# Optimization experiments

Measured on AMD Instinct MI355X. Metric: run time of the kernel, lower is better.

## Reference

```python
import jax, jax.numpy as jnp
import numpy as np

IN_CH = 256
NUM_CLASSES = 1
CONF_THR = 0.3
NMS_IOU = 0.2
ANCHOR_SIZES = (32.0, 64.0, 128.0)
ASPECTS = (0.5, 1.0, 2.0)
NUM_ANCHORS = len(ANCHOR_SIZES) * len(ASPECTS)  # 9
K_CAND = 1024   # top-score candidates fed to NMS per image
MAX_DET = 100   # max_output_size in source
BN_EPS = 1e-5


def _anchors():
    a = [[s * r / 224.0, s / r / 224.0] for s in ANCHOR_SIZES for r in ASPECTS]
    return jnp.asarray(a, jnp.float32)  # [A, 2] (w, h)


def _conv(x, w, b, pad):
    y = jax.lax.conv_general_dilated(x, w, (1, 1), [(pad, pad), (pad, pad)],
                                     dimension_numbers=('NCHW', 'OIHW', 'NCHW'))
    return y + b[None, :, None, None]


def _bn(x, g, b, m, v):
    inv = jax.lax.rsqrt(v + BN_EPS)
    return (x - m[None, :, None, None]) * (g * inv)[None, :, None, None] + b[None, :, None, None]


def _corners(b):
    return (b[..., 0] - b[..., 2] / 2, b[..., 1] - b[..., 3] / 2,
            b[..., 0] + b[..., 2] / 2, b[..., 1] + b[..., 3] / 2)


def _iou_one(box, boxes):
    # box: [4] cxcywh, boxes: [K,4] -> iou [K]
    ax1, ay1, ax2, ay2 = _corners(box)
    bx1, by1, bx2, by2 = _corners(boxes)
    iw = jnp.maximum(jnp.minimum(ax2, bx2) - jnp.maximum(ax1, bx1), 0.0)
    ih = jnp.maximum(jnp.minimum(ay2, by2) - jnp.maximum(ay1, by1), 0.0)
    inter = iw * ih
    union = (ax2 - ax1) * (ay2 - ay1) + (bx2 - bx1) * (by2 - by1) - inter
    return inter / (union + 1e-16)


def _nms(boxes, scores):
    # boxes [K,4], scores [K] -> kept boxes padded to [MAX_DET,4]
    s0 = jnp.where(scores > CONF_THR, scores, -1.0)

    def body(i, carry):
        s, out = carry
        j = jnp.argmax(s)
        ok = s[j] > 0.0
        box = boxes[j]
        iou = _iou_one(box, boxes)
        s_new = jnp.where(iou > NMS_IOU, -1.0, s).at[j].set(-1.0)
        s = jnp.where(ok, s_new, s)
        out = out.at[i].set(jnp.where(ok, box, jnp.zeros_like(box)))
        return s, out

    _, out = jax.lax.fori_loop(0, MAX_DET, body,
                               (s0, jnp.zeros((MAX_DET, 4), boxes.dtype)))
    return out


def _forward(features, w1, b1, g1, be1, m1, v1, w2, b2, g2, be2, m2, v2, wo, bo):
    x = jax.nn.relu(_bn(_conv(features, w1, b1, 1), g1, be1, m1, v1))
    x = jax.nn.relu(_bn(_conv(x, w2, b2, 1), g2, be2, m2, v2))
    p = _conv(x, wo, bo, 0)                      # [B, A*(5+C), H, W]
    B, _, H, W = p.shape
    p = p.reshape(B, NUM_ANCHORS, 5 + NUM_CLASSES, H, W).transpose(0, 3, 4, 1, 2)  # [B,H,W,A,5+C]
    obj = jax.nn.sigmoid(p[..., 4])
    anch = _anchors()
    gx = jnp.arange(W, dtype=p.dtype)[None, :, None]
    gy = jnp.arange(H, dtype=p.dtype)[:, None, None]
    px = (jax.nn.sigmoid(p[..., 0]) + gx) / W
    py = (jax.nn.sigmoid(p[..., 1]) + gy) / H
    pw = jnp.exp(p[..., 2]) * anch[:, 0]
    ph = jnp.exp(p[..., 3]) * anch[:, 1]
    boxes = jnp.stack([px, py, pw, ph], -1).reshape(B, -1, 4)
    if NUM_CLASSES > 1:
        scores = obj * jax.nn.sigmoid(p[..., 5:]).max(-1)
    else:
        scores = obj
    scores = scores.reshape(B, -1)

    def per_image(bx, sc):
        top_s, idx = jax.lax.top_k(sc, K_CAND)
        return _nms(bx[idx], top_s)

    return jax.vmap(per_image)(boxes, scores)    # [B, MAX_DET, 4]


def setup_inputs() -> dict:
    key = jax.random.key(0)
    ks = jax.random.split(key, 16)
    B = 32
    c1, c2 = IN_CH // 2, IN_CH // 4
    oc = NUM_ANCHORS * (5 + NUM_CLASSES)
    return {
        'features': jax.random.normal(ks[0], (B, IN_CH, 56, 56), jnp.float32),
        'w1': jax.random.normal(ks[1], (c1, IN_CH, 3, 3), jnp.float32) * 0.02,
        'b1': jax.random.normal(ks[2], (c1,), jnp.float32) * 0.02,
        'g1': 1.0 + 0.1 * jax.random.normal(ks[3], (c1,), jnp.float32),
        'be1': 0.1 * jax.random.normal(ks[4], (c1,), jnp.float32),
        'm1': 0.1 * jax.random.normal(ks[5], (c1,), jnp.float32),
        'v1': jax.random.uniform(ks[6], (c1,), jnp.float32, 0.5, 1.5),
        'w2': jax.random.normal(ks[7], (c2, c1, 3, 3), jnp.float32) * 0.03,
        'b2': jax.random.normal(ks[8], (c2,), jnp.float32) * 0.02,
        'g2': 1.0 + 0.1 * jax.random.normal(ks[9], (c2,), jnp.float32),
        'be2': 0.1 * jax.random.normal(ks[10], (c2,), jnp.float32),
        'm2': 0.1 * jax.random.normal(ks[11], (c2,), jnp.float32),
        'v2': jax.random.uniform(ks[12], (c2,), jnp.float32, 0.5, 1.5),
        'wo': jax.random.normal(ks[13], (oc, c2, 1, 1), jnp.float32) * 0.1,
        'bo': jax.random.normal(ks[14], (oc,), jnp.float32) * 0.05,
    }


def reference(features, w1, b1, g1, be1, m1, v1, w2, b2, g2, be2, m2, v2, wo, bo):
    return _forward(features, w1, b1, g1, be1, m1, v1, w2, b2, g2, be2, m2, v2, wo, bo)
```

## Files before the change

kernel.cpp:

```cpp
#include <hip/hip_runtime.h>
#include <math.h>
#include <stdint.h>

constexpr int BB   = 32;
constexpr int HW   = 3136;
constexpr int C0   = 256, C1 = 128, C2 = 64;
constexpr int NA   = 9;
constexpr int NCAND = HW * NA;
constexpr int KSEL  = 1024;
constexpr int MAXDET = 100;

typedef _Float16 half8 __attribute__((ext_vector_type(8)));
typedef _Float16 half4v __attribute__((ext_vector_type(4)));
typedef float    f32x4  __attribute__((ext_vector_type(4)));
typedef float    f32x16 __attribute__((ext_vector_type(16)));

__device__ __forceinline__ void g2l16(const void* g, void* l) {
    auto gp = reinterpret_cast<const __attribute__((address_space(1))) char*>(
        reinterpret_cast<uintptr_t>(g));
    auto lp = reinterpret_cast<__attribute__((address_space(3))) char*>(
        reinterpret_cast<uintptr_t>(l));
    __builtin_amdgcn_global_load_lds(gp, lp, 16, 0, 0);
}

__global__ void bn_prep(const float* __restrict__ g, const float* __restrict__ be,
                        const float* __restrict__ m, const float* __restrict__ v,
                        const float* __restrict__ cb,
                        float* __restrict__ scl, float* __restrict__ tb, int n) {
    int i = threadIdx.x;
    if (i < n) {
        float inv = 1.f / sqrtf(v[i] + 1e-5f);
        float s = g[i] * inv;
        scl[i] = s;
        tb[i] = be[i] + (cb[i] - m[i]) * s;
    }
}

__global__ void reorder_w6(const float* __restrict__ w, _Float16* __restrict__ wc,
                           int CIN, int COUT) {
    int i = blockIdx.x * 256 + threadIdx.x;
    int K = CIN * 9;
    if (i >= 2 * COUT * K) return;
    int ci  = i & 31;
    int row = (i >> 5) % (2 * COUT);
    int ch  = (i >> 5) / (2 * COUT);
    int pl  = row / COUT;
    int oc  = row - pl * COUT;
    int cg = ch / 9, r = ch - cg * 9;
    int cin = cg * 32 + ci;
    float v = w[oc * K + cin * 9 + r];
    _Float16 h = (_Float16)v;
    wc[i] = pl ? (_Float16)(v - (float)h) : h;
}

__global__ __launch_bounds__(256) void nchw_to_nhwc_split(
    const float* __restrict__ in, _Float16* __restrict__ hi, _Float16* __restrict__ lo)
{
    __shared__ float tile[64 * 68];
    const int pt = blockIdx.x * 64, ct = blockIdx.y * 64, b = blockIdx.z;
    const int t = threadIdx.x;
    const int r0 = t >> 4, cidx = (t & 15) * 4;
#pragma unroll
    for (int rr = 0; rr < 64; rr += 16) {
        int r = rr + r0;
        const float* src = in + ((size_t)(b * 256 + ct + r)) * HW + pt + cidx;
        float4 v = *(const float4*)src;
        float* d = &tile[r * 68 + cidx];
        d[0] = v.x; d[1] = v.y; d[2] = v.z; d[3] = v.w;
    }
    __syncthreads();
    const int p = t >> 2, c0 = (t & 3) * 16;
    size_t obase = ((size_t)(b * HW + pt + p)) * 256 + ct + c0;
    half8 h0, h1, l0, l1;
#pragma unroll
    for (int j = 0; j < 16; ++j) {
        float v = tile[(c0 + j) * 68 + p];
        _Float16 hh = (_Float16)v;
        _Float16 ll = (_Float16)(v - (float)hh);
        if (j < 8) { h0[j] = hh; l0[j] = ll; }
        else       { h1[j - 8] = hh; l1[j - 8] = ll; }
    }
    *(half8*)(hi + obase)     = h0;
    *(half8*)(hi + obase + 8) = h1;
    *(half8*)(lo + obase)     = l0;
    *(half8*)(lo + obase + 8) = l1;
}

template <int CIN, int COUT, int MINW, bool NHWC_OUT>
__global__ __launch_bounds__(256, MINW) void conv3x3_v10(
    const _Float16* __restrict__ xhi,
    const _Float16* __restrict__ xlo,
    const _Float16* __restrict__ wc,
    const _Float16* __restrict__ zbuf,
    const float* __restrict__ scl, const float* __restrict__ tb,
    _Float16* __restrict__ ohi,
    _Float16* __restrict__ olo,
    float* __restrict__ onchw)
{
    constexpr int K       = CIN * 9;
    constexpr int NCH     = K / 32;
    constexpr int WROWS   = 2 * COUT;
    constexpr int CHALVES = WROWS * 32;
    constexpr int WI      = WROWS / 64;
    constexpr int PI      = 2;
    constexpr int WOC     = COUT / 64;

    __shared__ __align__(16) _Float16 SP[128 * 64];
    __shared__ __align__(16) _Float16 SW[WROWS * 32];

    const int bid = blockIdx.x;
    const int swz = (bid & 7) * (gridDim.x >> 3) + (bid >> 3);
    const int b = swz / 25;
    const int pixBase = (swz - b * 25) * 128;
    const int bHW = b * HW;

    const int t = threadIdx.x, l = t & 63, w = t >> 6;

    const int cpix = (l & 7) ^ ((l >> 3) & 7);
    const int ppl = cpix >> 2, pq = cpix & 3;
    const _Float16* xsp = ppl ? xlo : xhi;
    int py[4], px[4];
    const _Float16* pbase[4];
#pragma unroll
    for (int i = 0; i < 4; ++i) {
        int p = w * 32 + i * 8 + (l >> 3);
        int pix = pixBase + p;
        py[i] = pix / 56; px[i] = pix - py[i] * 56;
        pbase[i] = xsp + (size_t)(bHW + pix) * CIN + pq * 8;
    }
    const int cw = (l & 3) ^ ((l >> 3) & 3);
    const _Float16* wbase = wc + ((size_t)(w * (WI * 16) + (l >> 2))) * 32 + cw * 8;

    const int wid = t >> 6;
    const int wp = wid & 1, wo = wid >> 1;
    const int lc = l & 31, lk = l >> 5;

    f32x16 acc[PI][WOC];
#pragma unroll
    for (int pi = 0; pi < PI; ++pi)
#pragma unroll
        for (int oi = 0; oi < WOC; ++oi) acc[pi][oi] = (f32x16)0.f;

    auto stage = [&](int ch) {
        int cg = ch / 9, r = ch - cg * 9;
        int ky = r / 3;
        int dy = ky - 1, dx = (r - ky * 3) - 1;
        int off = (dy * 56 + dx) * CIN + cg * 32;
#pragma unroll
        for (int i = 0; i < 4; ++i) {
            bool v = ((unsigned)(py[i] + dy) < 56u) && ((unsigned)(px[i] + dx) < 56u);
            const void* src = v ? (const void*)(pbase[i] + off) : (const void*)zbuf;
            g2l16(src, (void*)&SP[w * 2048 + i * 512]);
        }
        const _Float16* wsrc = wbase + (size_t)ch * CHALVES;
#pragma unroll
        for (int j = 0; j < WI; ++j)
            g2l16((const void*)(wsrc + j * 512), (void*)&SW[(w * WI + j) * 512]);
    };

    auto compute = [&]() {
#pragma unroll
        for (int ks = 0; ks < 2; ++ks) {
            half8 pb[PI][2];
#pragma unroll
            for (int pi = 0; pi < PI; ++pi) {
                int prw = wp * (PI * 32) + pi * 32 + lc;
                int key = prw & 7;
#pragma unroll
                for (int pl2 = 0; pl2 < 2; ++pl2) {
                    int c = pl2 * 4 + ks * 2 + lk;
                    pb[pi][pl2] = *(const half8*)&SP[prw * 64 + ((c ^ key) << 3)];
                }
            }
            half8 wa[WOC][2];
#pragma unroll
            for (int oi = 0; oi < WOC; ++oi)
#pragma unroll
                for (int pl2 = 0; pl2 < 2; ++pl2) {
                    int row = pl2 * COUT + wo * (WOC * 32) + oi * 32 + lc;
                    int c = ks * 2 + lk;
                    wa[oi][pl2] = *(const half8*)&SW[row * 32 + ((c ^ ((row >> 1) & 3)) << 3)];
                }
#pragma unroll
            for (int pi = 0; pi < PI; ++pi)
#pragma unroll
                for (int oi = 0; oi < WOC; ++oi) {
                    acc[pi][oi] = __builtin_amdgcn_mfma_f32_32x32x16_f16(wa[oi][0], pb[pi][0], acc[pi][oi], 0, 0, 0);
                    acc[pi][oi] = __builtin_amdgcn_mfma_f32_32x32x16_f16(wa[oi][0], pb[pi][1], acc[pi][oi], 0, 0, 0);
                    acc[pi][oi] = __builtin_amdgcn_mfma_f32_32x32x16_f16(wa[oi][1], pb[pi][0], acc[pi][oi], 0, 0, 0);
                }
        }
    };

    for (int ch = 0; ch < NCH; ++ch) {
        stage(ch);
        __syncthreads();
        compute();
        __syncthreads();
    }

#pragma unroll
    for (int pi = 0; pi < PI; ++pi) {
        const int pix = pixBase + wp * (PI * 32) + pi * 32 + lc;
        if (pix < HW) {
#pragma unroll
            for (int oi = 0; oi < WOC; ++oi) {
#pragma unroll
                for (int g = 0; g < 4; ++g) {
                    const int oc0 = wo * (WOC * 32) + oi * 32 + 8 * g + 4 * lk;
                    f32x4 s4 = *(const f32x4*)(scl + oc0);
                    f32x4 t4 = *(const f32x4*)(tb + oc0);
                    if constexpr (NHWC_OUT) {
                        half4v hh, ll;
#pragma unroll
                        for (int m2 = 0; m2 < 4; ++m2) {
                            float val = fmaxf(acc[pi][oi][g * 4 + m2] * s4[m2] + t4[m2], 0.f);
                            _Float16 h = (_Float16)val;
                            hh[m2] = h;
                            ll[m2] = (_Float16)(val - (float)h);
                        }
                        size_t o = ((size_t)(bHW + pix)) * COUT + oc0;
                        *(half4v*)(ohi + o) = hh;
                        *(half4v*)(olo + o) = ll;
                    } else {
#pragma unroll
                        for (int m2 = 0; m2 < 4; ++m2) {
                            float val = fmaxf(acc[pi][oi][g * 4 + m2] * s4[m2] + t4[m2], 0.f);
                            onchw[((size_t)(b * COUT + oc0 + m2)) * HW + pix] = val;
                        }
                    }
                }
            }
        }
    }
}

__global__ __launch_bounds__(256) void conv1x1_decode(
    const float* __restrict__ x2, const float* __restrict__ wo,
    const float* __restrict__ bo,
    float* __restrict__ boxes, float* __restrict__ scores)
{
    __shared__ float ws[64 * 56];
    for (int i = threadIdx.x; i < 54 * 64; i += 256) {
        int oc = i % 54, c = i / 54;
        ws[c * 56 + oc] = wo[oc * 64 + c];
    }
    __syncthreads();

    int u = blockIdx.x * 256 + threadIdx.x;
    int a = u % 9;
    int rest = u / 9;
    int quad = rest % 784;
    int b = rest / 784;
    int pix0 = quad * 4;
    int y = pix0 / 56;
    int x0 = pix0 - y * 56;

    const float* xb = x2 + (size_t)b * 64 * HW + pix0;
    float acc[5][4];
#pragma unroll
    for (int j = 0; j < 5; ++j)
#pragma unroll
        for (int p = 0; p < 4; ++p) acc[j][p] = 0.f;

#pragma unroll 8
    for (int c = 0; c < 64; ++c) {
        float4 xv = *(const float4*)(xb + c * HW);
#pragma unroll
        for (int j = 0; j < 5; ++j) {
            float w = ws[c * 56 + a * 6 + j];
            acc[j][0] += w * xv.x;
            acc[j][1] += w * xv.y;
            acc[j][2] += w * xv.z;
            acc[j][3] += w * xv.w;
        }
    }

    int si = a / 3, ri = a - si * 3;
    float sv = (float)(32 << si);
    float rv = 0.5f * (float)(1 << ri);
    float aw = (sv * rv) / 224.f;
    float ah = (sv / rv) / 224.f;
    float bo0 = bo[a * 6 + 0], bo1 = bo[a * 6 + 1], bo2 = bo[a * 6 + 2];
    float bo3 = bo[a * 6 + 3], bo4 = bo[a * 6 + 4];

#pragma unroll
    for (int p = 0; p < 4; ++p) {
        float p0 = acc[0][p] + bo0;
        float p1 = acc[1][p] + bo1;
        float p2 = acc[2][p] + bo2;
        float p3 = acc[3][p] + bo3;
        float p4 = acc[4][p] + bo4;
        float sx = 1.f / (1.f + expf(-p0));
        float sy = 1.f / (1.f + expf(-p1));
        float pxc = (sx + (float)(x0 + p)) / 56.f;
        float pyc = (sy + (float)y) / 56.f;
        float pw = expf(p2) * aw;
        float ph = expf(p3) * ah;
        float sc = 1.f / (1.f + expf(-p4));
        int n = (y * 56 + x0 + p) * 9 + a;
        float4 bx; bx.x = pxc; bx.y = pyc; bx.z = pw; bx.w = ph;
        *(float4*)&boxes[((size_t)b * NCAND + n) * 4] = bx;
        scores[(size_t)b * NCAND + n] = sc;
    }
}

__device__ __forceinline__ unsigned fkey(float f) {
    unsigned u = __float_as_uint(f);
    return (u & 0x80000000u) ? ~u : (u | 0x80000000u);
}

__global__ __launch_bounds__(1024) void topk_select(
    const float* __restrict__ scores, const float* __restrict__ boxes,
    float* __restrict__ cbox, float* __restrict__ csc, int* __restrict__ cidx)
{
    const int b = blockIdx.x, t = threadIdx.x;
    const float* sp = scores + (size_t)b * NCAND;
    const int lane = t & 63, w = t >> 6;

    __shared__ unsigned hist[256];
    __shared__ unsigned wsum[16];
    __shared__ unsigned s_sel, s_need, s_tot0, s_tot1;

    unsigned prefix = 0, maskSo = 0;
    int need = KSEL;

    for (int round = 0; round < 4; ++round) {
        int shift = 24 - round * 8;
        if (t < 256) hist[t] = 0;
        __syncthreads();
        for (int i = t; i < NCAND; i += 1024) {
            unsigned u = fkey(sp[i]);
            if ((u & maskSo) == prefix) atomicAdd(&hist[(u >> shift) & 255], 1u);
        }
        __syncthreads();
        if (t == 0) {
            int rem = need;
            unsigned sel = 0;
            for (int v = 255; v >= 0; --v) {
                int c = (int)hist[v];
                if (c >= rem) { sel = (unsigned)v; break; }
                rem -= c;
            }
            s_sel = sel; s_need = (unsigned)rem;
        }
        __syncthreads();
        prefix |= (s_sel << shift);
        maskSo |= (0xFFu << shift);
        need = (int)s_need;
        __syncthreads();
    }

    const unsigned cutoff = prefix;
    const unsigned needT = (unsigned)need;
    unsigned outBase = 0, tieBase = 0;
    const unsigned long long mlt = (1ull << lane) - 1ull;

    for (int c0 = 0; c0 < NCAND; c0 += 1024) {
        int i = c0 + t;
        bool valid = i < NCAND;
        float sc = valid ? sp[i] : 0.f;
        unsigned u = valid ? fkey(sc) : 0u;
        bool gt = valid && (u > cutoff);
        bool eq = valid && (u == cutoff);

        unsigned long long balE = __ballot(eq);
        unsigned lpE = (unsigned)__popcll(balE & mlt);
        if (lane == 0) wsum[w] = (unsigned)__popcll(balE);
        __syncthreads();
        if (t == 0) {
            unsigned run = 0;
            for (int k = 0; k < 16; ++k) { unsigned x = wsum[k]; wsum[k] = run; run += x; }
            s_tot1 = run;
        }
        __syncthreads();
        unsigned tieRank = tieBase + wsum[w] + lpE;
        bool take = gt || (eq && tieRank < needT);
        __syncthreads();

        unsigned long long balT = __ballot(take);
        unsigned lpT = (unsigned)__popcll(balT & mlt);
        if (lane == 0) wsum[w] = (unsigned)__popcll(balT);
        __syncthreads();
        if (t == 0) {
            unsigned run = 0;
            for (int k = 0; k < 16; ++k) { unsigned x = wsum[k]; wsum[k] = run; run += x; }
            s_tot0 = run;
        }
        __syncthreads();
        unsigned pos = outBase + wsum[w] + lpT;
        if (take) {
            float4 bx = *(const float4*)&boxes[((size_t)b * NCAND + i) * 4];
            *(float4*)&cbox[((size_t)b * KSEL + pos) * 4] = bx;
            csc[(size_t)b * KSEL + pos] = sc;
            cidx[(size_t)b * KSEL + pos] = i;
        }
        tieBase += s_tot1;
        outBase += s_tot0;
        __syncthreads();
    }
}

__global__ __launch_bounds__(64) void nms_wave(
    const float* __restrict__ cbox, const float* __restrict__ csc,
    const int* __restrict__ cidx, float* __restrict__ out)
{
    const int b = blockIdx.x, l = threadIdx.x;
    float cx[16], cy[16], w_[16], h_[16], s[16];
    int id[16];
#pragma unroll
    for (int j = 0; j < 16; ++j) {
        int ci = (b << 10) + (j << 6) + l;
        float4 bb = *(const float4*)&cbox[(size_t)ci * 4];
        float sc = csc[ci];
        cx[j] = bb.x; cy[j] = bb.y; w_[j] = bb.z; h_[j] = bb.w;
        s[j] = sc > 0.3f ? sc : -1.f;
        id[j] = cidx[ci];
    }
    float* ob = out + (size_t)b * MAXDET * 4;

    for (int it = 0; it < MAXDET; ++it) {
        float bs = s[0]; int bi = id[0];
        float bcx = cx[0], bcy = cy[0], bw = w_[0], bh = h_[0];
#pragma unroll
        for (int j = 1; j < 16; ++j) {
            bool tk = (s[j] > bs) || (s[j] == bs && id[j] < bi);
            if (tk) { bs = s[j]; bi = id[j]; bcx = cx[j]; bcy = cy[j]; bw = w_[j]; bh = h_[j]; }
        }
#pragma unroll
        for (int m2 = 1; m2 < 64; m2 <<= 1) {
            float os = __shfl_xor(bs, m2); int oi = __shfl_xor(bi, m2);
            float ox = __shfl_xor(bcx, m2), oy = __shfl_xor(bcy, m2);
            float ow = __shfl_xor(bw, m2), oh2 = __shfl_xor(bh, m2);
            bool tk = (os > bs) || (os == bs && oi < bi);
            if (tk) { bs = os; bi = oi; bcx = ox; bcy = oy; bw = ow; bh = oh2; }
        }
        if (bs <= 0.f) {
            for (int q = it * 4 + l; q < MAXDET * 4; q += 64) ob[q] = 0.f;
            break;
        }
        if (l == 0) {
            float4 o; o.x = bcx; o.y = bcy; o.z = bw; o.w = bh;
            *(float4*)&ob[it * 4] = o;
        }
        float wx1 = bcx - bw / 2.f, wy1 = bcy - bh / 2.f;
        float wx2 = bcx + bw / 2.f, wy2 = bcy + bh / 2.f;
        float war = (wx2 - wx1) * (wy2 - wy1);
#pragma unroll
        for (int j = 0; j < 16; ++j) {
            float jx1 = cx[j] - w_[j] / 2.f, jy1 = cy[j] - h_[j] / 2.f;
            float jx2 = cx[j] + w_[j] / 2.f, jy2 = cy[j] + h_[j] / 2.f;
            float iw = fminf(wx2, jx2) - fmaxf(wx1, jx1); iw = fmaxf(iw, 0.f);
            float ih = fminf(wy2, jy2) - fmaxf(wy1, jy1); ih = fmaxf(ih, 0.f);
            float inter = iw * ih;
            float jar = (jx2 - jx1) * (jy2 - jy1);
            float uni = war + jar - inter;
            if (inter / (uni + 1e-16f) > 0.2f) s[j] = -1.f;
        }
    }
}

extern "C" void kernel_launch(void* const* d_in, const int* in_sizes, int n_in,
                              void* d_out, int out_size, void* d_ws, size_t ws_size,
                              hipStream_t stream)
{
    const float* features = (const float*)d_in[0];
    const float* w1 = (const float*)d_in[1];
    const float* b1 = (const float*)d_in[2];
    const float* g1 = (const float*)d_in[3];
    const float* be1 = (const float*)d_in[4];
    const float* m1 = (const float*)d_in[5];
    const float* v1 = (const float*)d_in[6];
    const float* w2 = (const float*)d_in[7];
    const float* b2 = (const float*)d_in[8];
    const float* g2 = (const float*)d_in[9];
    const float* be2 = (const float*)d_in[10];
    const float* m2 = (const float*)d_in[11];
    const float* v2 = (const float*)d_in[12];
    const float* wo = (const float*)d_in[13];
    const float* bo = (const float*)d_in[14];

    char* ws = (char*)d_ws;
    size_t off = 0;
    auto alloc = [&](size_t bytes) {
        char* p = ws + off;
        off += (bytes + 255) / 256 * 256;
        return p;
    };

    _Float16* zbuf = (_Float16*)alloc(256);
    _Float16* w1c = (_Float16*)alloc((size_t)2 * C1 * 2304 * 2);
    _Float16* w2c = (_Float16*)alloc((size_t)2 * C2 * 1152 * 2);
    float* scl1 = (float*)alloc(C1 * 4);
    float* tb1  = (float*)alloc(C1 * 4);
    float* scl2 = (float*)alloc(C2 * 4);
    float* tb2  = (float*)alloc(C2 * 4);

    const size_t planeF = (size_t)BB * HW * C0 * 2;
    char* regB = alloc(2 * planeF);
    _Float16* fhi = (_Float16*)regB;
    _Float16* flo = (_Float16*)(regB + planeF);

    const size_t planeX1 = (size_t)BB * HW * C1 * 2;
    char* regC = alloc(2 * planeX1);
    _Float16* x1hi = (_Float16*)regC;
    _Float16* x1lo = (_Float16*)(regC + planeX1);

    float* x2     = (float*)regB;
    float* boxes  = (float*)(regB + 25690112);
    float* scores = (float*)(regB + 25690112 + 14450688);
    float* cbox = (float*)regC;
    float* csc  = (float*)(regC + 524288);
    int*   cidx = (int*)(regC + 524288 + 131072);

    hipMemsetAsync(zbuf, 0, 256, stream);
    bn_prep<<<1, 256, 0, stream>>>(g1, be1, m1, v1, b1, scl1, tb1, C1);
    bn_prep<<<1, 256, 0, stream>>>(g2, be2, m2, v2, b2, scl2, tb2, C2);
    reorder_w6<<<(2 * C1 * 2304 + 255) / 256, 256, 0, stream>>>(w1, w1c, C0, C1);
    reorder_w6<<<(2 * C2 * 1152 + 255) / 256, 256, 0, stream>>>(w2, w2c, C1, C2);

    nchw_to_nhwc_split<<<dim3(49, 4, BB), 256, 0, stream>>>(features, fhi, flo);

    conv3x3_v10<C0, C1, 4, true><<<800, 256, 0, stream>>>(
        fhi, flo, w1c, zbuf, scl1, tb1, x1hi, x1lo, nullptr);
    conv3x3_v10<C1, C2, 4, false><<<800, 256, 0, stream>>>(
        x1hi, x1lo, w2c, zbuf, scl2, tb2, nullptr, nullptr, x2);

    conv1x1_decode<<<(BB * 784 * NA) / 256, 256, 0, stream>>>(x2, wo, bo, boxes, scores);

    topk_select<<<BB, 1024, 0, stream>>>(scores, boxes, cbox, csc, cidx);
    nms_wave<<<BB, 64, 0, stream>>>(cbox, csc, cidx, (float*)d_out);
}
```

Before: 650.1 us.

## Use atomic compaction and warp-aggregated histograms in top-k select, merge prep kernels

```diff
diff --git a/kernel.cpp b/kernel.cpp
--- a/kernel.cpp
+++ b/kernel.cpp
@@ -23,24 +23,29 @@
     __builtin_amdgcn_global_load_lds(gp, lp, 16, 0, 0);
 }
 
-__global__ void bn_prep(const float* __restrict__ g, const float* __restrict__ be,
-                        const float* __restrict__ m, const float* __restrict__ v,
-                        const float* __restrict__ cb,
-                        float* __restrict__ scl, float* __restrict__ tb, int n) {
+__global__ void bn_prep2(const float* g1, const float* be1, const float* m1,
+                         const float* v1, const float* cb1,
+                         const float* g2, const float* be2, const float* m2,
+                         const float* v2, const float* cb2,
+                         float* scl1, float* tb1, float* scl2, float* tb2) {
     int i = threadIdx.x;
-    if (i < n) {
-        float inv = 1.f / sqrtf(v[i] + 1e-5f);
-        float s = g[i] * inv;
-        scl[i] = s;
-        tb[i] = be[i] + (cb[i] - m[i]) * s;
-    }
-}
-
-__global__ void reorder_w6(const float* __restrict__ w, _Float16* __restrict__ wc,
-                           int CIN, int COUT) {
-    int i = blockIdx.x * 256 + threadIdx.x;
+    if (i < C1) {
+        float inv = 1.f / sqrtf(v1[i] + 1e-5f);
+        float s = g1[i] * inv;
+        scl1[i] = s;
+        tb1[i] = be1[i] + (cb1[i] - m1[i]) * s;
+    }
+    if (i < C2) {
+        float inv = 1.f / sqrtf(v2[i] + 1e-5f);
+        float s = g2[i] * inv;
+        scl2[i] = s;
+        tb2[i] = be2[i] + (cb2[i] - m2[i]) * s;
+    }
+}
+
+__device__ __forceinline__ void reorder_one(const float* w, _Float16* wc,
+                                            int i, int CIN, int COUT) {
     int K = CIN * 9;
-    if (i >= 2 * COUT * K) return;
     int ci  = i & 31;
     int row = (i >> 5) % (2 * COUT);
     int ch  = (i >> 5) / (2 * COUT);
@@ -51,6 +56,15 @@
     float v = w[oc * K + cin * 9 + r];
     _Float16 h = (_Float16)v;
     wc[i] = pl ? (_Float16)(v - (float)h) : h;
+}
+
+__global__ void reorder_w_both(const float* __restrict__ w1, _Float16* __restrict__ w1c,
+                               const float* __restrict__ w2, _Float16* __restrict__ w2c) {
+    constexpr int N1 = 2 * C1 * C0 * 9;
+    constexpr int N2 = 2 * C2 * C1 * 9;
+    int i = blockIdx.x * 256 + threadIdx.x;
+    if (i < N1) reorder_one(w1, w1c, i, C0, C1);
+    else if (i < N1 + N2) reorder_one(w2, w2c, i - N1, C1, C2);
 }
 
 __global__ __launch_bounds__(256) void nchw_to_nhwc_split(
@@ -312,7 +326,8 @@
 
 __global__ __launch_bounds__(1024) void topk_select(
     const float* __restrict__ scores, const float* __restrict__ boxes,
-    float* __restrict__ cbox, float* __restrict__ csc, int* __restrict__ cidx)
+    float* __restrict__ cbox, float* __restrict__ csc, int* __restrict__ cidx,
+    int* __restrict__ ctrs)
 {
     const int b = blockIdx.x, t = threadIdx.x;
     const float* sp = scores + (size_t)b * NCAND;
@@ -320,7 +335,7 @@
 
     __shared__ unsigned hist[256];
     __shared__ unsigned wsum[16];
-    __shared__ unsigned s_sel, s_need, s_tot0, s_tot1;
+    __shared__ unsigned s_sel, s_need, s_tot1;
 
     unsigned prefix = 0, maskSo = 0;
     int need = KSEL;
@@ -329,9 +344,19 @@
         int shift = 24 - round * 8;
         if (t < 256) hist[t] = 0;
         __syncthreads();
-        for (int i = t; i < NCAND; i += 1024) {
-            unsigned u = fkey(sp[i]);
-            if ((u & maskSo) == prefix) atomicAdd(&hist[(u >> shift) & 255], 1u);
+        for (int i = t; i < NCAND + (1024 - NCAND % 1024); i += 1024) {
+            bool pred = i < NCAND;
+            unsigned u = pred ? fkey(sp[i]) : 0u;
+            pred = pred && ((u & maskSo) == prefix);
+            unsigned bin = (u >> shift) & 255;
+            unsigned long long active = __ballot(pred);
+            while (active) {
+                int leader = __ffsll((unsigned long long)active) - 1;
+                unsigned bl = __shfl(bin, leader);
+                unsigned long long match = __ballot(pred && bin == bl);
+                if (lane == leader) atomicAdd(&hist[bl], (unsigned)__popcll(match));
+                active &= ~match;
+            }
         }
         __syncthreads();
         if (t == 0) {
@@ -353,19 +378,26 @@
 
     const unsigned cutoff = prefix;
     const unsigned needT = (unsigned)need;
-    unsigned outBase = 0, tieBase = 0;
     const unsigned long long mlt = (1ull << lane) - 1ull;
 
+    for (int i = t; i < NCAND; i += 1024) {
+        unsigned u = fkey(sp[i]);
+        if (u > cutoff) {
+            int pos = atomicAdd(&ctrs[b], 1);
+            float4 bx = *(const float4*)&boxes[((size_t)b * NCAND + i) * 4];
+            *(float4*)&cbox[((size_t)b * KSEL + pos) * 4] = bx;
+            csc[(size_t)b * KSEL + pos] = sp[i];
+            cidx[(size_t)b * KSEL + pos] = i;
+        }
+    }
+
+    unsigned tieBase = 0;
     for (int c0 = 0; c0 < NCAND; c0 += 1024) {
         int i = c0 + t;
         bool valid = i < NCAND;
         float sc = valid ? sp[i] : 0.f;
-        unsigned u = valid ? fkey(sc) : 0u;
-        bool gt = valid && (u > cutoff);
-        bool eq = valid && (u == cutoff);
-
+        bool eq = valid && (fkey(sc) == cutoff);
         unsigned long long balE = __ballot(eq);
-        unsigned lpE = (unsigned)__popcll(balE & mlt);
         if (lane == 0) wsum[w] = (unsigned)__popcll(balE);
         __syncthreads();
         if (t == 0) {
@@ -374,30 +406,17 @@
             s_tot1 = run;
         }
         __syncthreads();
-        unsigned tieRank = tieBase + wsum[w] + lpE;
-        bool take = gt || (eq && tieRank < needT);
-        __syncthreads();
-
-        unsigned long long balT = __ballot(take);
-        unsigned lpT = (unsigned)__popcll(balT & mlt);
-        if (lane == 0) wsum[w] = (unsigned)__popcll(balT);
-        __syncthreads();
-        if (t == 0) {
-            unsigned run = 0;
-            for (int k = 0; k < 16; ++k) { unsigned x = wsum[k]; wsum[k] = run; run += x; }
-            s_tot0 = run;
-        }
-        __syncthreads();
-        unsigned pos = outBase + wsum[w] + lpT;
-        if (take) {
+        unsigned rank = tieBase + wsum[w] + (unsigned)__popcll(balE & mlt);
+        if (eq && rank < needT) {
+            int pos = atomicAdd(&ctrs[b], 1);
             float4 bx = *(const float4*)&boxes[((size_t)b * NCAND + i) * 4];
             *(float4*)&cbox[((size_t)b * KSEL + pos) * 4] = bx;
             csc[(size_t)b * KSEL + pos] = sc;
             cidx[(size_t)b * KSEL + pos] = i;
         }
         tieBase += s_tot1;
-        outBase += s_tot0;
-        __syncthreads();
+        __syncthreads();
+        if (tieBase >= needT) break;
     }
 }
 
@@ -489,6 +508,7 @@
     };
 
     _Float16* zbuf = (_Float16*)alloc(256);
+    int* ctrs = (int*)alloc(BB * 4);
     _Float16* w1c = (_Float16*)alloc((size_t)2 * C1 * 2304 * 2);
     _Float16* w2c = (_Float16*)alloc((size_t)2 * C2 * 1152 * 2);
     float* scl1 = (float*)alloc(C1 * 4);
@@ -514,10 +534,13 @@
     int*   cidx = (int*)(regC + 524288 + 131072);
 
     hipMemsetAsync(zbuf, 0, 256, stream);
-    bn_prep<<<1, 256, 0, stream>>>(g1, be1, m1, v1, b1, scl1, tb1, C1);
-    bn_prep<<<1, 256, 0, stream>>>(g2, be2, m2, v2, b2, scl2, tb2, C2);
-    reorder_w6<<<(2 * C1 * 2304 + 255) / 256, 256, 0, stream>>>(w1, w1c, C0, C1);
-    reorder_w6<<<(2 * C2 * 1152 + 255) / 256, 256, 0, stream>>>(w2, w2c, C1, C2);
+    hipMemsetAsync(ctrs, 0, BB * 4, stream);
+    bn_prep2<<<1, 256, 0, stream>>>(g1, be1, m1, v1, b1, g2, be2, m2, v2, b2,
+                                    scl1, tb1, scl2, tb2);
+    {
+        int total = 2 * C1 * 2304 + 2 * C2 * 1152;
+        reorder_w_both<<<(total + 255) / 256, 256, 0, stream>>>(w1, w1c, w2, w2c);
+    }
 
     nchw_to_nhwc_split<<<dim3(49, 4, BB), 256, 0, stream>>>(features, fhi, flo);
 
@@ -528,6 +551,6 @@
 
     conv1x1_decode<<<(BB * 784 * NA) / 256, 256, 0, stream>>>(x2, wo, bo, boxes, scores);
 
-    topk_select<<<BB, 1024, 0, stream>>>(scores, boxes, cbox, csc, cidx);
+    topk_select<<<BB, 1024, 0, stream>>>(scores, boxes, cbox, csc, cidx, ctrs);
     nms_wave<<<BB, 64, 0, stream>>>(cbox, csc, cidx, (float*)d_out);
 }
```

Result: slower. 756.9 us (+16.4%).
